# Performance work log

Measured on AMD Instinct MI355X. Metric: run time of the kernel, lower is better.

The kernel has to match this reference:

```python
import jax, jax.numpy as jnp
import numpy as np

N_FREQS = 6  # PositionEmbedding default used by LISA


def setup_inputs() -> dict:
    key = jax.random.key(0)
    ks = jax.random.split(key, 8)
    B, L, N, D, H = 8, 32768, 2048, 64, 256
    in_dim = 1 * (2 * N_FREQS + 1) + 3 * D  # 13 + 192 = 205

    def w(k, i, o):
        return jax.random.normal(k, (i, o), jnp.float32) * (1.0 / np.sqrt(i))

    return {
        "coord": jax.random.uniform(ks[0], (B, L, 1), jnp.float32),
        "latent": jax.random.normal(ks[1], (B, N, D), jnp.float32),
        "W0": w(ks[2], in_dim, H), "b0": jnp.zeros((H,), jnp.float32),
        "W1": w(ks[3], H, H), "b1": jnp.zeros((H,), jnp.float32),
        "W2": w(ks[4], H, H), "b2": jnp.zeros((H,), jnp.float32),
        "W3": w(ks[5], H, H), "b3": jnp.zeros((H,), jnp.float32),
        "W4": w(ks[6], H, 1), "b4": jnp.zeros((1,), jnp.float32),
    }


def reference(coord, latent, W0, b0, W1, b1, W2, b2, W3, b3, W4, b4):
    B, N, D = latent.shape
    # feat_unfold: concat shifted-prev / self / shifted-next along channels
    feat = jnp.swapaxes(latent, 1, 2)                                   # [B, D, N]
    feat_prev = jnp.concatenate([feat[:, :, :1], feat[:, :, :-1]], axis=2)
    feat_next = jnp.concatenate([feat[:, :, 1:], feat[:, :, -1:]], axis=2)
    feat = jnp.concatenate([feat_prev, feat, feat_next], axis=1)        # [B, 3D, N]

    # grid_sample(bilinear, padding_mode='border', align_corners=False) on a
    # 1-row image: y coordinate 0 hits row 0 exactly, so only x interpolates.
    # torch mapping: ix = ((gx + 1) * W - 1) / 2 with gx = coord*2 - 1
    ix = coord[..., 0] * N - 0.5                                        # [B, L]
    x0 = jnp.floor(ix)
    t = ix - x0                                                         # lerp weight
    i0 = jnp.clip(x0.astype(jnp.int32), 0, N - 1)                       # border clamp
    i1 = jnp.clip(x0.astype(jnp.int32) + 1, 0, N - 1)
    f0 = jnp.take_along_axis(feat, i0[:, None, :], axis=2)              # [B, 3D, L]
    f1 = jnp.take_along_axis(feat, i1[:, None, :], axis=2)
    sampled = (1.0 - t)[:, None, :] * f0 + t[:, None, :] * f1
    sampled = jnp.swapaxes(sampled, 1, 2)                               # [B, L, 3D]

    # positional encoding: [x, sin(f x), cos(f x) for f in 1,2,4,8,16,32]
    freqs = 2.0 ** jnp.arange(N_FREQS, dtype=jnp.float32)
    ang = coord * freqs                                                 # [B, L, 6]
    pe = jnp.stack([jnp.sin(ang), jnp.cos(ang)], axis=-1)
    pe = pe.reshape(ang.shape[0], ang.shape[1], 2 * N_FREQS)            # [B, L, 12]

    inp = jnp.concatenate([coord, pe, sampled], axis=-1)                # [B, L, 205]

    h = jax.nn.relu(inp @ W0 + b0)
    h = jax.nn.relu(h @ W1 + b1)
    h = jax.nn.relu(h @ W2 + b2)
    h = jax.nn.relu(h @ W3 + b3)
    return h @ W4 + b4                                                  # [B, L, 1]
```

## Files before the change

### kernel.cpp

```cpp
#include <hip/hip_runtime.h>
#include <hip/hip_bf16.h>

typedef unsigned short ushort_t;
typedef unsigned int uint_t;
typedef __attribute__((ext_vector_type(8))) short short8;
typedef __attribute__((ext_vector_type(4))) float float4v;
typedef __attribute__((ext_vector_type(4))) uint_t uint4v;

#define NLAT 2048
#define DLAT 64

#define PW_BASE 128
#define PW0_OFF 0
#define PW1_OFF 57344
#define PW2_OFF 122880
#define PW3_OFF 188416

__device__ __forceinline__ float b2f(ushort_t u) {
  union { uint_t i; float f; } v; v.i = ((uint_t)u) << 16; return v.f;
}
__device__ __forceinline__ ushort_t f2b(float f) {
  uint_t x = __float_as_uint(f);
  uint_t r = (x + 0x7fffu + ((x >> 16) & 1u)) >> 16;
  return (ushort_t)r;
}
__device__ __forceinline__ uint_t pack2(float lo, float hi) {
  float2 t; t.x = lo; t.y = hi;
  union { __hip_bfloat162 h; uint_t u; } cv;
  cv.h = __float22bfloat162_rn(t);
  return cv.u;
}
__device__ __forceinline__ int imin(int a, int b) { return a < b ? a : b; }
__device__ __forceinline__ int imax(int a, int b) { return a > b ? a : b; }

__device__ __forceinline__ float ldv(const float* p, long i)    { return p[i]; }
__device__ __forceinline__ float ldv(const ushort_t* p, long i) { return b2f(p[i]); }
__device__ __forceinline__ void stv(float* p, long i, float v)    { p[i] = v; }
__device__ __forceinline__ void stv(ushort_t* p, long i, float v) { p[i] = f2b(v); }

__device__ __forceinline__ float4 load4f(const float* p) { return *(const float4*)p; }
__device__ __forceinline__ float4 load4f(const ushort_t* p) {
  uint2 u = *(const uint2*)p;
  float4 r;
  r.x = b2f((ushort_t)(u.x & 0xffffu)); r.y = b2f((ushort_t)(u.x >> 16));
  r.z = b2f((ushort_t)(u.y & 0xffffu)); r.w = b2f((ushort_t)(u.y >> 16));
  return r;
}

__device__ __forceinline__ void async_copy16(const ushort_t* g, ushort_t* l) {
  __builtin_amdgcn_global_load_lds(
      (const __attribute__((address_space(1))) void*)g,
      (__attribute__((address_space(3))) void*)l, 16, 0, 0);
}

template <int KT>
__device__ __forceinline__ void stage_q_t(ushort_t* dst, const ushort_t* src, int tid) {
#pragma unroll
  for (int r = 0; r < KT; ++r) {
    int i = tid + (r << 8);
    async_copy16(src + (size_t)i * 8, dst + (size_t)i * 8);
  }
}
__device__ __forceinline__ void stage_gi(int gi, ushort_t* dst,
                                         const ushort_t* __restrict__ pw, int tid) {
  int layer = gi >> 2, q = gi & 3;
  if (layer == 0) {
    stage_q_t<7>(dst, pw + PW0_OFF + q * 7 * 2048, tid);
  } else {
    int loff = (layer == 1) ? PW1_OFF : (layer == 2) ? PW2_OFF : PW3_OFF;
    stage_q_t<8>(dst, pw + loff + q * 8 * 2048, tid);
  }
}

__global__ void detect_mode(const ushort_t* __restrict__ lat, int* __restrict__ flag) {
  if (threadIdx.x == 0) *flag = 0;
  __syncthreads();
  int big = 0;
  for (int i = threadIdx.x; i < 1024; i += 64) {
    float v = b2f(lat[i]);
    if (!(fabsf(v) < 1e5f)) big = 1;
  }
  if (__any(big) && threadIdx.x == 0) *flag = 1;
}

template <typename TI>
__global__ void pack_w_t(const TI* __restrict__ W0, const TI* __restrict__ W1,
                         const TI* __restrict__ W2, const TI* __restrict__ W3,
                         ushort_t* __restrict__ pw, const int* __restrict__ flag, int want)
{
  if (*flag != want) return;
  int g = blockIdx.x * blockDim.x + threadIdx.x;
  if (g >= 31 * 1024) return;
  int lane = g & 63, q = lane >> 4;
  int mt   = (g >> 6) & 15;
  int ktg  = g >> 10;
  const TI* W; ushort_t* dst; int kt, KT; bool isw0 = false;
  if (ktg < 7)       { W = W0; dst = pw + PW0_OFF; kt = ktg;      KT = 7; isw0 = true; }
  else if (ktg < 15) { W = W1; dst = pw + PW1_OFF; kt = ktg - 7;  KT = 8; }
  else if (ktg < 23) { W = W2; dst = pw + PW2_OFF; kt = ktg - 15; KT = 8; }
  else               { W = W3; dst = pw + PW3_OFF; kt = ktg - 23; KT = 8; }
  int col = mt * 16 + (lane & 15);
  uint_t words[4];
#pragma unroll
  for (int h = 0; h < 4; ++h) {
    ushort_t vv[2];
#pragma unroll
    for (int e = 0; e < 2; ++e) {
      int j = 2 * h + e;
      int f = 32 * kt + 16 * (j >> 2) + 4 * q + (j & 3);
      int row = f;
      if (isw0) row = (f < 192) ? (13 + f) : (f == 192 ? 0 : (f <= 204 ? f - 192 : -1));
      vv[e] = (row >= 0) ? f2b(ldv(W, (long)row * 256 + col)) : (ushort_t)0;
    }
    words[h] = (uint_t)vv[0] | ((uint_t)vv[1] << 16);
  }
  uint4 o; o.x = words[0]; o.y = words[1]; o.z = words[2]; o.w = words[3];
  *(uint4*)(dst + ((size_t)(mt * KT + kt) * 64 + lane) * 8) = o;
}

template <int KT>
__device__ __forceinline__ void run_layer(int base, float4v (&acc)[16][2],
                                          const uint4v (&hu)[8][2],
                                          ushort_t (*wbuf)[16384],
                                          const ushort_t* __restrict__ pw,
                                          int tid, int lane)
{
#pragma unroll
  for (int qq = 0; qq < 4; ++qq) {
    const int gi = base + qq;
    if (gi + 1 < 16) stage_gi(gi + 1, wbuf[(gi + 1) & 1], pw, tid);
    const ushort_t* buf = wbuf[gi & 1];
#pragma unroll
    for (int m = 0; m < 4; ++m) {
      acc[qq * 4 + m][0] = (float4v){0.f, 0.f, 0.f, 0.f};
      acc[qq * 4 + m][1] = (float4v){0.f, 0.f, 0.f, 0.f};
    }
    short8 aL[2], aH[2];
    aL[0] = *(const short8*)&buf[((size_t)(0 * KT + 0) * 64 + lane) * 8];
    aL[1] = *(const short8*)&buf[((size_t)(1 * KT + 0) * 64 + lane) * 8];
#pragma unroll
    for (int kt = 0; kt < KT; ++kt) {
      aH[0] = *(const short8*)&buf[((size_t)(2 * KT + kt) * 64 + lane) * 8];
      aH[1] = *(const short8*)&buf[((size_t)(3 * KT + kt) * 64 + lane) * 8];
      short8 b0 = __builtin_bit_cast(short8, hu[kt][0]);
      short8 b1 = __builtin_bit_cast(short8, hu[kt][1]);
      acc[qq * 4 + 0][0] = __builtin_amdgcn_mfma_f32_16x16x32_bf16(aL[0], b0, acc[qq * 4 + 0][0], 0, 0, 0);
      acc[qq * 4 + 0][1] = __builtin_amdgcn_mfma_f32_16x16x32_bf16(aL[0], b1, acc[qq * 4 + 0][1], 0, 0, 0);
      acc[qq * 4 + 1][0] = __builtin_amdgcn_mfma_f32_16x16x32_bf16(aL[1], b0, acc[qq * 4 + 1][0], 0, 0, 0);
      acc[qq * 4 + 1][1] = __builtin_amdgcn_mfma_f32_16x16x32_bf16(aL[1], b1, acc[qq * 4 + 1][1], 0, 0, 0);
      if (kt + 1 < KT) {
        aL[0] = *(const short8*)&buf[((size_t)(0 * KT + kt + 1) * 64 + lane) * 8];
        aL[1] = *(const short8*)&buf[((size_t)(1 * KT + kt + 1) * 64 + lane) * 8];
      }
      acc[qq * 4 + 2][0] = __builtin_amdgcn_mfma_f32_16x16x32_bf16(aH[0], b0, acc[qq * 4 + 2][0], 0, 0, 0);
      acc[qq * 4 + 2][1] = __builtin_amdgcn_mfma_f32_16x16x32_bf16(aH[0], b1, acc[qq * 4 + 2][1], 0, 0, 0);
      acc[qq * 4 + 3][0] = __builtin_amdgcn_mfma_f32_16x16x32_bf16(aH[1], b0, acc[qq * 4 + 3][0], 0, 0, 0);
      acc[qq * 4 + 3][1] = __builtin_amdgcn_mfma_f32_16x16x32_bf16(aH[1], b1, acc[qq * 4 + 3][1], 0, 0, 0);
    }
    __syncthreads();
  }
}

__device__ __forceinline__ void convert_layer(float4v (&acc)[16][2], uint4v (&hu)[8][2],
                                              const float* bwl, int q)
{
#pragma unroll
  for (int mt = 0; mt < 16; ++mt) {
    float4 b4 = *(const float4*)&bwl[mt * 16 + 4 * q];
#pragma unroll
    for (int g = 0; g < 2; ++g) {
      float v0 = fmaxf(acc[mt][g][0] + b4.x, 0.f);
      float v1 = fmaxf(acc[mt][g][1] + b4.y, 0.f);
      float v2 = fmaxf(acc[mt][g][2] + b4.z, 0.f);
      float v3 = fmaxf(acc[mt][g][3] + b4.w, 0.f);
      hu[mt >> 1][g][(mt & 1) * 2 + 0] = pack2(v0, v1);
      hu[mt >> 1][g][(mt & 1) * 2 + 1] = pack2(v2, v3);
    }
  }
}

template <typename TI>
__global__ __launch_bounds__(256, 2) void lisa_fused_t(
    const TI* __restrict__ coord, const TI* __restrict__ latent,
    const TI* __restrict__ bias0, const TI* __restrict__ bias1,
    const TI* __restrict__ bias2, const TI* __restrict__ bias3,
    const TI* __restrict__ W4,    const TI* __restrict__ b4,
    const ushort_t* __restrict__ pw, TI* __restrict__ out,
    const int* __restrict__ flag, int want)
{
  if (*flag != want) return;
  __shared__ __align__(16) ushort_t wbuf[2][16384];
  __shared__ __align__(16) float bw[4 * 256 + 256 + 1];

  const int tid  = threadIdx.x;
  const int lane = tid & 63, q = lane >> 4, m15 = lane & 15;
  const int wv   = tid >> 6;
  const long pbase = (long)blockIdx.x * 128 + wv * 32 + m15;

  stage_gi(0, wbuf[0], pw, tid);
  for (int i = tid; i < 1281; i += 256) {
    float v;
    if (i < 256)       v = ldv(bias0, i);
    else if (i < 512)  v = ldv(bias1, i - 256);
    else if (i < 768)  v = ldv(bias2, i - 512);
    else if (i < 1024) v = ldv(bias3, i - 768);
    else if (i < 1280) v = ldv(W4, i - 1024);
    else               v = ldv(b4, 0);
    bw[i] = v;
  }

  uint4v hu[8][2];
#pragma unroll
  for (int g = 0; g < 2; ++g) {
    long p = pbase + g * 16;
    float c   = ldv(coord, p);
    float ixv = c * 2048.0f - 0.5f;
    float x0f = floorf(ixv);
    float t   = ixv - x0f;
    int   x0  = (int)x0f;
    int   i0  = imin(imax(x0, 0), NLAT - 1);
    int   i1  = imin(imax(x0 + 1, 0), NLAT - 1);
    float w0 = 1.0f - t, w1 = t;
    int rows0[3] = { imax(i0 - 1, 0), i0, imin(i0 + 1, NLAT - 1) };
    int rows1[3] = { imax(i1 - 1, 0), i1, imin(i1 + 1, NLAT - 1) };
    const TI* lat = latent + (size_t)(p >> 15) * (NLAT * DLAT);
#pragma unroll
    for (int tb = 0; tb < 12; ++tb) {
      int region = tb >> 2;
      int d0 = 16 * (tb & 3) + 4 * q;
      float4 a = load4f(lat + (long)rows0[region] * DLAT + d0);
      float4 b = load4f(lat + (long)rows1[region] * DLAT + d0);
      hu[tb >> 1][g][(tb & 1) * 2 + 0] = pack2(w0 * a.x + w1 * b.x, w0 * a.y + w1 * b.y);
      hu[tb >> 1][g][(tb & 1) * 2 + 1] = pack2(w0 * a.z + w1 * b.z, w0 * a.w + w1 * b.w);
    }
    float pv[4];
#pragma unroll
    for (int s = 0; s < 4; ++s) {
      int f = 192 + 4 * q + s;
      float v = 0.0f;
      if (f == 192) v = c;
      else if (f <= 204) {
        int i = f - 193;
        float fr = (float)(1 << (i >> 1));
        float ang = c * fr;
        v = (i & 1) ? __cosf(ang) : __sinf(ang);
      }
      pv[s] = v;
    }
    hu[6][g][0] = pack2(pv[0], pv[1]);
    hu[6][g][1] = pack2(pv[2], pv[3]);
    hu[6][g][2] = 0; hu[6][g][3] = 0;
  }
  __syncthreads();

  float4v acc[16][2];

  run_layer<7>( 0, acc, hu, wbuf, pw, tid, lane);
  convert_layer(acc, hu, bw + 0 * 256, q);
  run_layer<8>( 4, acc, hu, wbuf, pw, tid, lane);
  convert_layer(acc, hu, bw + 1 * 256, q);
  run_layer<8>( 8, acc, hu, wbuf, pw, tid, lane);
  convert_layer(acc, hu, bw + 2 * 256, q);
  run_layer<8>(12, acc, hu, wbuf, pw, tid, lane);

  float partial0 = 0.f, partial1 = 0.f;
#pragma unroll
  for (int mt = 0; mt < 16; ++mt) {
    float4 b3v = *(const float4*)&bw[3 * 256 + mt * 16 + 4 * q];
    float4 w4v = *(const float4*)&bw[1024 + mt * 16 + 4 * q];
    float v;
    v = fmaxf(acc[mt][0][0] + b3v.x, 0.f); partial0 += v * w4v.x;
    v = fmaxf(acc[mt][0][1] + b3v.y, 0.f); partial0 += v * w4v.y;
    v = fmaxf(acc[mt][0][2] + b3v.z, 0.f); partial0 += v * w4v.z;
    v = fmaxf(acc[mt][0][3] + b3v.w, 0.f); partial0 += v * w4v.w;
    v = fmaxf(acc[mt][1][0] + b3v.x, 0.f); partial1 += v * w4v.x;
    v = fmaxf(acc[mt][1][1] + b3v.y, 0.f); partial1 += v * w4v.y;
    v = fmaxf(acc[mt][1][2] + b3v.z, 0.f); partial1 += v * w4v.z;
    v = fmaxf(acc[mt][1][3] + b3v.w, 0.f); partial1 += v * w4v.w;
  }
  partial0 += __shfl_xor(partial0, 16, 64);
  partial0 += __shfl_xor(partial0, 32, 64);
  partial1 += __shfl_xor(partial1, 16, 64);
  partial1 += __shfl_xor(partial1, 32, 64);
  if (lane < 16) {
    float bb = bw[1280];
    stv(out, pbase,      partial0 + bb);
    stv(out, pbase + 16, partial1 + bb);
  }
}

extern "C" void kernel_launch(void* const* d_in, const int* in_sizes, int n_in,
                              void* d_out, int out_size, void* d_ws, size_t ws_size,
                              hipStream_t stream) {
  int* flag = (int*)d_ws;
  ushort_t* pw = (ushort_t*)d_ws + PW_BASE;

  detect_mode<<<1, 64, 0, stream>>>((const ushort_t*)d_in[1], flag);

  pack_w_t<float><<<62, 512, 0, stream>>>(
      (const float*)d_in[2], (const float*)d_in[4], (const float*)d_in[6],
      (const float*)d_in[8], pw, flag, 1);
  lisa_fused_t<float><<<2048, 256, 0, stream>>>(
      (const float*)d_in[0], (const float*)d_in[1],
      (const float*)d_in[3], (const float*)d_in[5], (const float*)d_in[7],
      (const float*)d_in[9], (const float*)d_in[10], (const float*)d_in[11],
      pw, (float*)d_out, flag, 1);

  pack_w_t<ushort_t><<<62, 512, 0, stream>>>(
      (const ushort_t*)d_in[2], (const ushort_t*)d_in[4], (const ushort_t*)d_in[6],
      (const ushort_t*)d_in[8], pw, flag, 0);
  lisa_fused_t<ushort_t><<<2048, 256, 0, stream>>>(
      (const ushort_t*)d_in[0], (const ushort_t*)d_in[1],
      (const ushort_t*)d_in[3], (const ushort_t*)d_in[5], (const ushort_t*)d_in[7],
      (const ushort_t*)d_in[9], (const ushort_t*)d_in[10], (const ushort_t*)d_in[11],
      pw, (ushort_t*)d_out, flag, 0);
}
```

Measured before the change: 225.7 us.

## Stage only half of weight chunks in LDS, stream other half from global

After: 256.4 us. 1.14x slower.

```diff
diff --git a/kernel.cpp b/kernel.cpp
--- a/kernel.cpp
+++ b/kernel.cpp
@@ -54,21 +54,19 @@
 }
 
 template <int KT>
-__device__ __forceinline__ void stage_q_t(ushort_t* dst, const ushort_t* src, int tid) {
-#pragma unroll
-  for (int r = 0; r < KT; ++r) {
-    int i = tid + (r << 8);
+__device__ __forceinline__ void stage_h(ushort_t* dst, const ushort_t* src, int tid) {
+  int n = KT * 128;
+  for (int i = tid; i < n; i += 256)
     async_copy16(src + (size_t)i * 8, dst + (size_t)i * 8);
-  }
 }
 __device__ __forceinline__ void stage_gi(int gi, ushort_t* dst,
                                          const ushort_t* __restrict__ pw, int tid) {
-  int layer = gi >> 2, q = gi & 3;
+  int layer = gi >> 2, qq = gi & 3;
   if (layer == 0) {
-    stage_q_t<7>(dst, pw + PW0_OFF + q * 7 * 2048, tid);
+    stage_h<7>(dst, pw + PW0_OFF + (size_t)qq * 4 * 7 * 512, tid);
   } else {
     int loff = (layer == 1) ? PW1_OFF : (layer == 2) ? PW2_OFF : PW3_OFF;
-    stage_q_t<8>(dst, pw + loff + q * 8 * 2048, tid);
+    stage_h<8>(dst, pw + loff + (size_t)qq * 4 * 8 * 512, tid);
   }
 }
 
@@ -121,27 +119,33 @@
 template <int KT>
 __device__ __forceinline__ void run_layer(int base, float4v (&acc)[16][2],
                                           const uint4v (&hu)[8][2],
-                                          ushort_t (*wbuf)[16384],
-                                          const ushort_t* __restrict__ pw,
+                                          ushort_t (*wbuf)[8192],
+                                          const ushort_t* __restrict__ pw, int loff,
                                           int tid, int lane)
 {
 #pragma unroll
   for (int qq = 0; qq < 4; ++qq) {
     const int gi = base + qq;
     if (gi + 1 < 16) stage_gi(gi + 1, wbuf[(gi + 1) & 1], pw, tid);
-    const ushort_t* buf = wbuf[gi & 1];
+    const ushort_t* buf  = wbuf[gi & 1];
+    const ushort_t* gsrc = pw + loff + (size_t)(qq * 4 + 2) * KT * 512;
 #pragma unroll
     for (int m = 0; m < 4; ++m) {
       acc[qq * 4 + m][0] = (float4v){0.f, 0.f, 0.f, 0.f};
       acc[qq * 4 + m][1] = (float4v){0.f, 0.f, 0.f, 0.f};
     }
-    short8 aL[2], aH[2];
-    aL[0] = *(const short8*)&buf[((size_t)(0 * KT + 0) * 64 + lane) * 8];
-    aL[1] = *(const short8*)&buf[((size_t)(1 * KT + 0) * 64 + lane) * 8];
+    short8 aL[2], aH[2], aHn[2];
+    aL[0]  = *(const short8*)&buf[((size_t)(0 * KT + 0) * 64 + lane) * 8];
+    aL[1]  = *(const short8*)&buf[((size_t)(1 * KT + 0) * 64 + lane) * 8];
+    aHn[0] = *(const short8*)&gsrc[((size_t)(0 * KT + 0) * 64 + lane) * 8];
+    aHn[1] = *(const short8*)&gsrc[((size_t)(1 * KT + 0) * 64 + lane) * 8];
 #pragma unroll
     for (int kt = 0; kt < KT; ++kt) {
-      aH[0] = *(const short8*)&buf[((size_t)(2 * KT + kt) * 64 + lane) * 8];
-      aH[1] = *(const short8*)&buf[((size_t)(3 * KT + kt) * 64 + lane) * 8];
+      aH[0] = aHn[0]; aH[1] = aHn[1];
+      if (kt + 1 < KT) {
+        aHn[0] = *(const short8*)&gsrc[((size_t)(0 * KT + kt + 1) * 64 + lane) * 8];
+        aHn[1] = *(const short8*)&gsrc[((size_t)(1 * KT + kt + 1) * 64 + lane) * 8];
+      }
       short8 b0 = __builtin_bit_cast(short8, hu[kt][0]);
       short8 b1 = __builtin_bit_cast(short8, hu[kt][1]);
       acc[qq * 4 + 0][0] = __builtin_amdgcn_mfma_f32_16x16x32_bf16(aL[0], b0, acc[qq * 4 + 0][0], 0, 0, 0);
@@ -189,7 +193,7 @@
     const int* __restrict__ flag, int want)
 {
   if (*flag != want) return;
-  __shared__ __align__(16) ushort_t wbuf[2][16384];
+  __shared__ __align__(16) ushort_t wbuf[2][8192];
   __shared__ __align__(16) float bw[4 * 256 + 256 + 1];
 
   const int tid  = threadIdx.x;
@@ -255,13 +259,13 @@
 
   float4v acc[16][2];
 
-  run_layer<7>( 0, acc, hu, wbuf, pw, tid, lane);
+  run_layer<7>( 0, acc, hu, wbuf, pw, PW0_OFF, tid, lane);
   convert_layer(acc, hu, bw + 0 * 256, q);
-  run_layer<8>( 4, acc, hu, wbuf, pw, tid, lane);
+  run_layer<8>( 4, acc, hu, wbuf, pw, PW1_OFF, tid, lane);
   convert_layer(acc, hu, bw + 1 * 256, q);
-  run_layer<8>( 8, acc, hu, wbuf, pw, tid, lane);
+  run_layer<8>( 8, acc, hu, wbuf, pw, PW2_OFF, tid, lane);
   convert_layer(acc, hu, bw + 2 * 256, q);
-  run_layer<8>(12, acc, hu, wbuf, pw, tid, lane);
+  run_layer<8>(12, acc, hu, wbuf, pw, PW3_OFF, tid, lane);
 
   float partial0 = 0.f, partial1 = 0.f;
 #pragma unroll
```
